# Kernel optimization log

Hardware: AMD Instinct MI355X
Metric: run time of the kernel (lower is better)

## Reference

```python
import jax, jax.numpy as jnp
import numpy as np

D_MODEL = 512
N_HEADS = 8
D_HEAD = D_MODEL // N_HEADS
MAX_LEN = 5000


def _make_pe():
    # sinusoidal table for relative positions -MAX_LEN..+MAX_LEN
    pos = np.arange(-MAX_LEN, MAX_LEN + 1, dtype=np.float32)[:, None]
    div = np.exp(np.arange(0, D_MODEL, 2, dtype=np.float32) * (-np.log(10000.0) / D_MODEL))
    pe = np.zeros((2 * MAX_LEN + 1, D_MODEL), dtype=np.float32)
    pe[:, 0::2] = np.sin(pos * div)
    pe[:, 1::2] = np.cos(pos * div)
    return jnp.asarray(pe)


def setup_inputs() -> dict:
    key = jax.random.key(0)
    ks = jax.random.split(key, 10)
    B, S = 8, 512
    xavier = lambda k: jax.random.uniform(k, (D_MODEL, D_MODEL), jnp.float32,
                                          -np.sqrt(6.0 / (2 * D_MODEL)), np.sqrt(6.0 / (2 * D_MODEL)))
    return {
        "x": jax.random.normal(ks[0], (B, S, D_MODEL), jnp.float32),
        "wq": xavier(ks[1]), "bq": jnp.zeros((D_MODEL,), jnp.float32),
        "wk": xavier(ks[2]), "bk": jnp.zeros((D_MODEL,), jnp.float32),
        "wv": xavier(ks[3]), "bv": jnp.zeros((D_MODEL,), jnp.float32),
        "wo": xavier(ks[4]), "bo": jnp.zeros((D_MODEL,), jnp.float32),
        "wr": xavier(ks[5]),
        "u": jnp.zeros((N_HEADS, D_HEAD), jnp.float32),
        "v_bias": jnp.zeros((N_HEADS, D_HEAD), jnp.float32),
        "pe": _make_pe(),
    }


def reference(x, wq, bq, wk, bk, wv, bv, wo, bo, wr, u, v_bias, pe):
    B, S, D = x.shape
    H, dh = N_HEADS, D_HEAD
    scale = dh ** -0.5

    # projections (torch Linear: x @ W.T + b) -> [B, H, S, dh]
    def proj(w, b):
        return (x @ w.T + b).reshape(B, S, H, dh).transpose(0, 2, 1, 3)
    q = proj(wq, bq)
    k = proj(wk, bk)
    v = proj(wv, bv)

    # relative position encodings: rel[i,j] = pe[clip(j-i) + MAX_LEN]
    pos = jnp.arange(S)
    rel_idx = jnp.clip(pos[None, :] - pos[:, None], -MAX_LEN, MAX_LEN) + MAX_LEN
    rel_pos = pe[rel_idx]                              # [S, S, D]
    rel_proj = (rel_pos @ wr.T).reshape(S, S, H, dh)   # [S, S, H, dh]
    rel_proj = rel_proj.transpose(2, 0, 1, 3)          # [H, S, S, dh]

    content = jnp.einsum('bhid,bhjd->bhij', q + u[None, :, None, :], k)
    position = jnp.einsum('bhid,hijd->bhij', q + v_bias[None, :, None, :], rel_proj)
    attn = jax.nn.softmax((content + position) * scale, axis=-1)

    out = jnp.einsum('bhij,bhjd->bhid', attn, v)       # [B, H, S, dh]
    out = out.transpose(0, 2, 1, 3).reshape(B, S, D)
    return out @ wo.T + bo
```

## Files before the change

### kernel.cpp

```cpp
#include <hip/hip_runtime.h>
#include <math.h>

#define DM 512
#define NH 8
#define DH 64
#define SEQ 512
#define BATCH 8
#define MR 1023
#define PE_OFF 4489

typedef float4 f4;
typedef __attribute__((ext_vector_type(8))) short bf16x8;
typedef __attribute__((ext_vector_type(4))) float f32x4;
typedef __attribute__((ext_vector_type(8))) unsigned short u16x8;
typedef __attribute__((ext_vector_type(4))) unsigned short u16x4;

__device__ __forceinline__ unsigned short f2bf(float f) {
    unsigned x = __float_as_uint(f);
    unsigned r = x + 0x7fffu + ((x >> 16) & 1u);
    return (unsigned short)(r >> 16);
}
__device__ __forceinline__ float bf2f(unsigned short h) {
    return __uint_as_float(((unsigned)h) << 16);
}
__device__ __forceinline__ f32x4 mfma16(bf16x8 a, bf16x8 b, f32x4 c) {
    return __builtin_amdgcn_mfma_f32_16x16x32_bf16(a, b, c, 0, 0, 0);
}

__device__ __forceinline__ void cvt8(const float* __restrict__ src,
                                     unsigned short* __restrict__ hi,
                                     unsigned short* __restrict__ lo, int i) {
    f4 a = *(const f4*)&src[i];
    f4 b = *(const f4*)&src[i + 4];
    float v[8] = {a.x, a.y, a.z, a.w, b.x, b.y, b.z, b.w};
    u16x8 h, l;
#pragma unroll
    for (int j = 0; j < 8; ++j) {
        unsigned short hb = f2bf(v[j]);
        h[j] = hb;
        l[j] = f2bf(v[j] - bf2f(hb));
    }
    *(u16x8*)&hi[i] = h;
    *(u16x8*)&lo[i] = l;
}

__global__ __launch_bounds__(256) void cvt_all_kernel(
    const float* __restrict__ x,
    const float* __restrict__ w0, const float* __restrict__ w1,
    const float* __restrict__ w2, const float* __restrict__ w3,
    const float* __restrict__ w4, const float* __restrict__ pe,
    unsigned short* __restrict__ xh, unsigned short* __restrict__ xl,
    unsigned short* __restrict__ wb,
    unsigned short* __restrict__ peh, unsigned short* __restrict__ pel)
{
    const int bid = blockIdx.x, tid = threadIdx.x;
    if (bid < 1024) {
        cvt8(x, xh, xl, (bid * 256 + tid) * 8);
    } else if (bid < 1664) {
        const int wsel = (bid - 1024) >> 7;
        const float* src = (wsel == 0) ? w0 : (wsel == 1) ? w1 :
                           (wsel == 2) ? w2 : (wsel == 3) ? w3 : w4;
        unsigned short* hi = wb + (size_t)wsel * 524288;
        cvt8(src, hi, hi + 262144, (((bid - 1024) & 127) * 256 + tid) * 8);
    } else {
        const int i = ((bid - 1664) * 256 + tid) * 8;
        if (i < 523776) cvt8(pe, peh, pel, i);
    }
}

__device__ __forceinline__ void gemm_core128(
    const unsigned short* __restrict__ Ah, const unsigned short* __restrict__ Al,
    const unsigned short* __restrict__ Wh, const unsigned short* __restrict__ Wl,
    int m0, int n0, f32x4 acc[4][2],
    unsigned short* LAh, unsigned short* LAl,
    unsigned short* LBh, unsigned short* LBl)
{
    const int tid = threadIdx.x;
    const int lane = tid & 63, wid = tid >> 6;
    const int wm = (wid >> 1) << 6, wn = (wid & 1) << 5;
    const int ar = tid >> 1, ac = (tid & 1) << 4;
    const int br = tid >> 2, bc = (tid & 3) << 3;
    const int fr = lane & 15, g = lane >> 4;

#pragma unroll
    for (int i = 0; i < 4; ++i)
#pragma unroll
        for (int j = 0; j < 2; ++j)
            acc[i][j] = (f32x4){0.f, 0.f, 0.f, 0.f};

    const size_t arow = (size_t)(m0 + ar) * DM + ac;
    const size_t wrow = (size_t)(n0 + br) * DM + bc;

    for (int k0 = 0; k0 < DM; k0 += 32) {
        u16x8 a0 = *(const u16x8*)&Ah[arow + k0];
        u16x8 a1 = *(const u16x8*)&Ah[arow + k0 + 8];
        u16x8 a2 = *(const u16x8*)&Al[arow + k0];
        u16x8 a3 = *(const u16x8*)&Al[arow + k0 + 8];
        u16x8 b0 = *(const u16x8*)&Wh[wrow + k0];
        u16x8 b1 = *(const u16x8*)&Wl[wrow + k0];
        if (k0) __syncthreads();
        *(u16x8*)&LAh[ar * 40 + ac] = a0;
        *(u16x8*)&LAh[ar * 40 + ac + 8] = a1;
        *(u16x8*)&LAl[ar * 40 + ac] = a2;
        *(u16x8*)&LAl[ar * 40 + ac + 8] = a3;
        *(u16x8*)&LBh[br * 40 + bc] = b0;
        *(u16x8*)&LBl[br * 40 + bc] = b1;
        __syncthreads();

        bf16x8 a_h[4], a_l[4], b_h[2], b_l[2];
#pragma unroll
        for (int mi = 0; mi < 4; ++mi) {
            a_h[mi] = *(const bf16x8*)&LAh[(wm + (mi << 4) + fr) * 40 + (g << 3)];
            a_l[mi] = *(const bf16x8*)&LAl[(wm + (mi << 4) + fr) * 40 + (g << 3)];
        }
#pragma unroll
        for (int ni = 0; ni < 2; ++ni) {
            b_h[ni] = *(const bf16x8*)&LBh[(wn + (ni << 4) + fr) * 40 + (g << 3)];
            b_l[ni] = *(const bf16x8*)&LBl[(wn + (ni << 4) + fr) * 40 + (g << 3)];
        }
#pragma unroll
        for (int mi = 0; mi < 4; ++mi)
#pragma unroll
            for (int ni = 0; ni < 2; ++ni) {
                acc[mi][ni] = mfma16(a_h[mi], b_h[ni], acc[mi][ni]);
                acc[mi][ni] = mfma16(a_h[mi], b_l[ni], acc[mi][ni]);
                acc[mi][ni] = mfma16(a_l[mi], b_h[ni], acc[mi][ni]);
            }
    }
}

#define GEMM_LDS \
    __shared__ unsigned short LAh[128 * 40], LAl[128 * 40]; \
    __shared__ unsigned short LBh[64 * 40], LBl[64 * 40];

__global__ __launch_bounds__(256) void qkv_kernel(
    const unsigned short* __restrict__ xh, const unsigned short* __restrict__ xl,
    const unsigned short* __restrict__ wb,
    const float* __restrict__ bq, const float* __restrict__ bk,
    const float* __restrict__ bv, const float* __restrict__ u,
    unsigned short* __restrict__ qh, unsigned short* __restrict__ ql,
    unsigned short* __restrict__ kh, unsigned short* __restrict__ kl,
    unsigned short* __restrict__ vth, unsigned short* __restrict__ vtl)
{
    GEMM_LDS
    const int wsel = blockIdx.x >> 3;
    const int n0 = (blockIdx.x & 7) << 6, m0 = blockIdx.y << 7;
    const unsigned short* Wh = wb + (size_t)wsel * 524288;
    const unsigned short* Wl = Wh + 262144;
    f32x4 acc[4][2];
    gemm_core128(xh, xl, Wh, Wl, m0, n0, acc, LAh, LAl, LBh, LBl);

    const int tid = threadIdx.x, lane = tid & 63, wid = tid >> 6;
    const int wm = (wid >> 1) << 6, wn = (wid & 1) << 5;
    const int fr = lane & 15, g = lane >> 4;
    const float* bias = (wsel == 0) ? bq : (wsel == 1) ? bk : bv;

    if (wsel < 2) {
        unsigned short* oh = (wsel == 0) ? qh : kh;
        unsigned short* ol = (wsel == 0) ? ql : kl;
#pragma unroll
        for (int ni = 0; ni < 2; ++ni) {
            const int n_g = n0 + wn + (ni << 4) + fr;
            float bvv = bias[n_g] + ((wsel == 0) ? u[n_g] : 0.f);
            const int h = n_g >> 6, d = n_g & 63;
#pragma unroll
            for (int mi = 0; mi < 4; ++mi)
#pragma unroll
                for (int r = 0; r < 4; ++r) {
                    const int m_g = m0 + wm + (mi << 4) + (g << 2) + r;
                    const int b = m_g >> 9, s = m_g & 511;
                    const float val = acc[mi][ni][r] + bvv;
                    const size_t o = ((size_t)(b * NH + h) * SEQ + s) * DH + d;
                    const unsigned short hb = f2bf(val);
                    oh[o] = hb;
                    ol[o] = f2bf(val - bf2f(hb));
                }
        }
    } else {
#pragma unroll
        for (int ni = 0; ni < 2; ++ni) {
            const int n_g = n0 + wn + (ni << 4) + fr;
            const float bvv = bias[n_g];
            const int h = n_g >> 6, d = n_g & 63;
#pragma unroll
            for (int mi = 0; mi < 4; ++mi) {
                const int m_b = m0 + wm + (mi << 4) + (g << 2);
                const int b = m_b >> 9, s = m_b & 511;
                u16x4 hv, lv;
#pragma unroll
                for (int r = 0; r < 4; ++r) {
                    const float val = acc[mi][ni][r] + bvv;
                    hv[r] = f2bf(val);
                    lv[r] = f2bf(val - bf2f(hv[r]));
                }
                const size_t o = ((size_t)(b * NH + h) * DH + d) * SEQ + s;
                *(u16x4*)&vth[o] = hv;
                *(u16x4*)&vtl[o] = lv;
            }
        }
    }
}

__global__ __launch_bounds__(256) void rm_kernel(
    const unsigned short* __restrict__ peh, const unsigned short* __restrict__ pel,
    const unsigned short* __restrict__ wrh, const unsigned short* __restrict__ wrl,
    const float* __restrict__ u, const float* __restrict__ vb,
    unsigned short* __restrict__ rmh, unsigned short* __restrict__ rml,
    float* __restrict__ rc)
{
    GEMM_LDS
    const int n0 = blockIdx.x << 6, m0 = blockIdx.y << 7;
    f32x4 acc[4][2];
    gemm_core128(peh, pel, wrh, wrl, m0, n0, acc, LAh, LAl, LBh, LBl);

    const int tid = threadIdx.x, lane = tid & 63, wid = tid >> 6;
    const int wm = (wid >> 1) << 6, wn = (wid & 1) << 5;
    const int fr = lane & 15, g = lane >> 4;
    const int h = n0 >> 6;

    float part[4][4];
    float wgt[2];
#pragma unroll
    for (int ni = 0; ni < 2; ++ni) {
        const int d = wn + (ni << 4) + fr;
        wgt[ni] = vb[(h << 6) + d] - u[(h << 6) + d];
    }
#pragma unroll
    for (int mi = 0; mi < 4; ++mi)
#pragma unroll
        for (int r = 0; r < 4; ++r) part[mi][r] = 0.f;

#pragma unroll
    for (int ni = 0; ni < 2; ++ni) {
        const int n_g = n0 + wn + (ni << 4) + fr;
        const int d = n_g & 63;
#pragma unroll
        for (int mi = 0; mi < 4; ++mi)
#pragma unroll
            for (int r = 0; r < 4; ++r) {
                const int dd = m0 + wm + (mi << 4) + (g << 2) + r;
                const float val = acc[mi][ni][r];
                const size_t o = (((size_t)h << 10) + dd) * DH + d;
                const unsigned short hb = f2bf(val);
                rmh[o] = hb;
                rml[o] = f2bf(val - bf2f(hb));
                part[mi][r] = fmaf(wgt[ni], val, part[mi][r]);
            }
    }

    __syncthreads();
    float* cbuf = (float*)LAh;
#pragma unroll
    for (int mi = 0; mi < 4; ++mi)
#pragma unroll
        for (int r = 0; r < 4; ++r) {
            float v = part[mi][r];
#pragma unroll
            for (int off = 8; off; off >>= 1) v += __shfl_xor(v, off, 16);
            if (fr == 0)
                cbuf[((wid & 1) << 7) + wm + (mi << 4) + (g << 2) + r] = v;
        }
    __syncthreads();
    if (tid < 128)
        rc[((size_t)h << 10) + m0 + tid] = cbuf[tid] + cbuf[128 + tid];
}

__global__ __launch_bounds__(256) void out_kernel(
    const unsigned short* __restrict__ cth, const unsigned short* __restrict__ ctl,
    const unsigned short* __restrict__ woh, const unsigned short* __restrict__ wol,
    const float* __restrict__ bo, float* __restrict__ out)
{
    GEMM_LDS
    const int n0 = blockIdx.x << 6, m0 = blockIdx.y << 7;
    f32x4 acc[4][2];
    gemm_core128(cth, ctl, woh, wol, m0, n0, acc, LAh, LAl, LBh, LBl);

    const int tid = threadIdx.x, lane = tid & 63, wid = tid >> 6;
    const int wm = (wid >> 1) << 6, wn = (wid & 1) << 5;
    const int fr = lane & 15, g = lane >> 4;
#pragma unroll
    for (int ni = 0; ni < 2; ++ni) {
        const int n_g = n0 + wn + (ni << 4) + fr;
        const float bvv = bo[n_g];
#pragma unroll
        for (int mi = 0; mi < 4; ++mi)
#pragma unroll
            for (int r = 0; r < 4; ++r) {
                const int m_g = m0 + wm + (mi << 4) + (g << 2) + r;
                out[(size_t)m_g * DM + n_g] = acc[mi][ni][r] + bvv;
            }
    }
}

__global__ __launch_bounds__(256) void attn_kernel(
    const unsigned short* __restrict__ qh_g, const unsigned short* __restrict__ ql_g,
    const unsigned short* __restrict__ kh_g, const unsigned short* __restrict__ kl_g,
    const unsigned short* __restrict__ vh_g, const unsigned short* __restrict__ vl_g,
    const unsigned short* __restrict__ rmh, const unsigned short* __restrict__ rml,
    const float* __restrict__ rc,
    unsigned short* __restrict__ cth, unsigned short* __restrict__ ctl)
{
    __shared__ unsigned short Kh[64][72], Kl[64][72], Vh[64][72], Vl[64][72];
    __shared__ unsigned short Pdd[4][16][84];
    __shared__ unsigned short Pth[4][16][72];

    const int tid = threadIdx.x;
    const int lane = tid & 63, wid = tid >> 6;
    const int g = lane >> 4, c = lane & 15;
    const int i0 = blockIdx.x << 6;
    const int h = blockIdx.y, b = blockIdx.z;
    const int R0 = i0 + (wid << 4);
    const size_t bh = (size_t)(b * NH + h) * (SEQ * DH);

    const int srow = tid >> 3;
    const int sch = (tid & 7) << 3;

    bf16x8 qhf[2], qlf[2];
#pragma unroll
    for (int ks = 0; ks < 2; ++ks) {
        const size_t qo = bh + (size_t)(R0 + c) * DH + (ks << 5) + (g << 3);
        qhf[ks] = *(const bf16x8*)&qh_g[qo];
        qlf[ks] = *(const bf16x8*)&ql_g[qo];
    }

    f32x4 Oacc[4];
#pragma unroll
    for (int nf = 0; nf < 4; ++nf) Oacc[nf] = (f32x4){0.f, 0.f, 0.f, 0.f};
    float m_r[4] = {-3e38f, -3e38f, -3e38f, -3e38f};
    float l_r[4] = {0.f, 0.f, 0.f, 0.f};

    const float* rch = rc + (h << 10);
    const unsigned short* rmhh = rmh + ((size_t)h << 16);
    const unsigned short* rmlh = rml + ((size_t)h << 16);

    u16x8 p0, p1, p2, p3, p4, p5, p6, p7;
    {
        const size_t kb = bh + (size_t)srow * DH + sch;
        p0 = *(const u16x8*)&kh_g[kb];
        p1 = *(const u16x8*)&kh_g[kb + 32 * DH];
        p2 = *(const u16x8*)&kl_g[kb];
        p3 = *(const u16x8*)&kl_g[kb + 32 * DH];
        const size_t vb_ = bh + (size_t)srow * SEQ + sch;
        p4 = *(const u16x8*)&vh_g[vb_];
        p5 = *(const u16x8*)&vh_g[vb_ + 32 * SEQ];
        p6 = *(const u16x8*)&vl_g[vb_];
        p7 = *(const u16x8*)&vl_g[vb_ + 32 * SEQ];
    }

    for (int jt = 0; jt < 8; ++jt) {
        const int j0 = jt << 6;
        __syncthreads();
        *(u16x8*)&Kh[srow][sch] = p0;
        *(u16x8*)&Kh[srow + 32][sch] = p1;
        *(u16x8*)&Kl[srow][sch] = p2;
        *(u16x8*)&Kl[srow + 32][sch] = p3;
        *(u16x8*)&Vh[srow][sch] = p4;
        *(u16x8*)&Vh[srow + 32][sch] = p5;
        *(u16x8*)&Vl[srow][sch] = p6;
        *(u16x8*)&Vl[srow + 32][sch] = p7;
        __syncthreads();
        if (jt < 7) {
            const int jn = j0 + 64;
            const size_t kb = bh + (size_t)(jn + srow) * DH + sch;
            p0 = *(const u16x8*)&kh_g[kb];
            p1 = *(const u16x8*)&kh_g[kb + 32 * DH];
            p2 = *(const u16x8*)&kl_g[kb];
            p3 = *(const u16x8*)&kl_g[kb + 32 * DH];
            const size_t vb_ = bh + (size_t)srow * SEQ + jn + sch;
            p4 = *(const u16x8*)&vh_g[vb_];
            p5 = *(const u16x8*)&vh_g[vb_ + 32 * SEQ];
            p6 = *(const u16x8*)&vl_g[vb_];
            p7 = *(const u16x8*)&vl_g[vb_ + 32 * SEQ];
        }

        __builtin_amdgcn_s_setprio(1);
        f32x4 accs[4];
#pragma unroll
        for (int nf = 0; nf < 4; ++nf) accs[nf] = (f32x4){0.f, 0.f, 0.f, 0.f};
#pragma unroll
        for (int ks = 0; ks < 2; ++ks)
#pragma unroll
            for (int nf = 0; nf < 4; ++nf) {
                bf16x8 b_h = *(const bf16x8*)&Kh[(nf << 4) + c][(ks << 5) + (g << 3)];
                bf16x8 b_l = *(const bf16x8*)&Kl[(nf << 4) + c][(ks << 5) + (g << 3)];
                accs[nf] = mfma16(qhf[ks], b_h, accs[nf]);
                accs[nf] = mfma16(qhf[ks], b_l, accs[nf]);
                accs[nf] = mfma16(qlf[ks], b_h, accs[nf]);
            }

        const int base_g = j0 - R0 + 496;
#pragma unroll
        for (int f = 0; f < 5; ++f) {
            f32x4 ap = (f32x4){0.f, 0.f, 0.f, 0.f};
#pragma unroll
            for (int ks = 0; ks < 2; ++ks) {
                const size_t ro = (size_t)(base_g + (f << 4) + c) * DH
                                + (ks << 5) + (g << 3);
                bf16x8 b_h = *(const bf16x8*)&rmhh[ro];
                bf16x8 b_l = *(const bf16x8*)&rmlh[ro];
                ap = mfma16(qhf[ks], b_h, ap);
                ap = mfma16(qhf[ks], b_l, ap);
                ap = mfma16(qlf[ks], b_h, ap);
            }
            const float rcv = rch[base_g + (f << 4) + c];
#pragma unroll
            for (int r = 0; r < 4; ++r)
                Pdd[wid][(g << 2) + r][(f << 4) + c] = f2bf(ap[r] + rcv);
        }
        __builtin_amdgcn_s_setprio(0);

#pragma unroll
        for (int r = 0; r < 4; ++r) {
            const int irow = (g << 2) + r;
            float sc[4];
#pragma unroll
            for (int nf = 0; nf < 4; ++nf) {
                const int ddl = (nf << 4) + c - irow + 15;
                sc[nf] = (accs[nf][r] + bf2f(Pdd[wid][irow][ddl])) * 0.125f;
            }
            float mt = fmaxf(fmaxf(sc[0], sc[1]), fmaxf(sc[2], sc[3]));
#pragma unroll
            for (int off = 8; off; off >>= 1) mt = fmaxf(mt, __shfl_xor(mt, off, 16));
            const float mn = fmaxf(m_r[r], mt);
            const float alpha = __expf(m_r[r] - mn);
            m_r[r] = mn;
            float rs = 0.f;
#pragma unroll
            for (int nf = 0; nf < 4; ++nf) {
                const float p = __expf(sc[nf] - mn);
                Pth[wid][irow][(nf << 4) + c] = f2bf(p);
                rs += p;
            }
#pragma unroll
            for (int off = 8; off; off >>= 1) rs += __shfl_xor(rs, off, 16);
            l_r[r] = l_r[r] * alpha + rs;
#pragma unroll
            for (int nf = 0; nf < 4; ++nf) Oacc[nf][r] *= alpha;
        }

        __builtin_amdgcn_s_setprio(1);
#pragma unroll
        for (int ks = 0; ks < 2; ++ks) {
            bf16x8 ph = *(const bf16x8*)&Pth[wid][c][(ks << 5) + (g << 3)];
#pragma unroll
            for (int nf = 0; nf < 4; ++nf) {
                bf16x8 v_h = *(const bf16x8*)&Vh[(nf << 4) + c][(ks << 5) + (g << 3)];
                bf16x8 v_l = *(const bf16x8*)&Vl[(nf << 4) + c][(ks << 5) + (g << 3)];
                Oacc[nf] = mfma16(ph, v_h, Oacc[nf]);
                Oacc[nf] = mfma16(ph, v_l, Oacc[nf]);
            }
        }
        __builtin_amdgcn_s_setprio(0);
    }

    float inv[4];
#pragma unroll
    for (int r = 0; r < 4; ++r) inv[r] = 1.f / l_r[r];
#pragma unroll
    for (int nf = 0; nf < 4; ++nf)
#pragma unroll
        for (int r = 0; r < 4; ++r) {
            const float val = Oacc[nf][r] * inv[r];
            const int s = R0 + (g << 2) + r;
            const int d = (h << 6) + (nf << 4) + c;
            const size_t o = ((size_t)(b * SEQ) + s) * DM + d;
            const unsigned short hb = f2bf(val);
            cth[o] = hb;
            ctl[o] = f2bf(val - bf2f(hb));
        }
}

extern "C" void kernel_launch(void* const* d_in, const int* in_sizes, int n_in,
                              void* d_out, int out_size, void* d_ws, size_t ws_size,
                              hipStream_t stream)
{
    const float* x  = (const float*)d_in[0];
    const float* wq = (const float*)d_in[1];
    const float* bq = (const float*)d_in[2];
    const float* wk = (const float*)d_in[3];
    const float* bk = (const float*)d_in[4];
    const float* wv = (const float*)d_in[5];
    const float* bv = (const float*)d_in[6];
    const float* wo = (const float*)d_in[7];
    const float* bo = (const float*)d_in[8];
    const float* wr = (const float*)d_in[9];
    const float* u  = (const float*)d_in[10];
    const float* vb = (const float*)d_in[11];
    const float* pe = (const float*)d_in[12];
    float* out = (float*)d_out;
    unsigned short* us = (unsigned short*)d_ws;

    unsigned short* xh  = us;
    unsigned short* xl  = us + 2097152;
    unsigned short* wb  = us + 4194304;
    unsigned short* peh = us + 6815744;
    unsigned short* pel = us + 7340032;
    unsigned short* qh  = us + 7864320;
    unsigned short* ql  = us + 9961472;
    unsigned short* kh  = us + 12058624;
    unsigned short* kl  = us + 14155776;
    unsigned short* vth = us + 16252928;
    unsigned short* vtl = us + 18350080;
    unsigned short* rmh = us + 20447232;
    unsigned short* rml = us + 20971520;
    unsigned short* cth = us + 21495808;
    unsigned short* ctl = us + 23592960;
    float* rc = (float*)(us + 25690112);

    unsigned short* woh = wb + 3 * 524288;
    unsigned short* wol = woh + 262144;
    unsigned short* wrh = wb + 4 * 524288;
    unsigned short* wrl = wrh + 262144;

    dim3 blk(256);
    cvt_all_kernel<<<1920, blk, 0, stream>>>(x, wq, wk, wv, wo, wr,
                                             pe + (size_t)PE_OFF * DM,
                                             xh, xl, wb, peh, pel);
    qkv_kernel<<<dim3(24, 32), blk, 0, stream>>>(xh, xl, wb, bq, bk, bv, u,
                                                 qh, ql, kh, kl, vth, vtl);
    rm_kernel<<<dim3(8, 8), blk, 0, stream>>>(peh, pel, wrh, wrl, u, vb,
                                              rmh, rml, rc);
    attn_kernel<<<dim3(8, 8, 8), blk, 0, stream>>>(qh, ql, kh, kl, vth, vtl,
                                                   rmh, rml, rc, cth, ctl);
    out_kernel<<<dim3(8, 32), blk, 0, stream>>>(cth, ctl, woh, wol, bo, out);
}
```

Baseline: 127.6 us.

## Fuse QKV and relative-position projections into one launch; split P into hi/lo for PV

Merges the relative-position projection GEMM into the QKV projection kernel as extra blocks of a single grid, removing a separate launch and letting the small rm GEMM overlap with QKV work. Separately, the attention kernel now keeps softmax probabilities in fp32 shared memory and splits them into bf16 hi/lo parts, adding a third MFMA per PV step for better precision. The precision change adds MFMA work, conversion ALU and LDS usage in the attention inner loop.

```diff
diff --git a/kernel.cpp b/kernel.cpp
--- a/kernel.cpp
+++ b/kernel.cpp
@@ -133,26 +133,90 @@
     __shared__ unsigned short LAh[128 * 40], LAl[128 * 40]; \
     __shared__ unsigned short LBh[64 * 40], LBl[64 * 40];
 
-__global__ __launch_bounds__(256) void qkv_kernel(
+__global__ __launch_bounds__(256) void qkv_rm_kernel(
     const unsigned short* __restrict__ xh, const unsigned short* __restrict__ xl,
     const unsigned short* __restrict__ wb,
+    const unsigned short* __restrict__ peh, const unsigned short* __restrict__ pel,
     const float* __restrict__ bq, const float* __restrict__ bk,
     const float* __restrict__ bv, const float* __restrict__ u,
+    const float* __restrict__ vb,
     unsigned short* __restrict__ qh, unsigned short* __restrict__ ql,
     unsigned short* __restrict__ kh, unsigned short* __restrict__ kl,
-    unsigned short* __restrict__ vth, unsigned short* __restrict__ vtl)
+    unsigned short* __restrict__ vth, unsigned short* __restrict__ vtl,
+    unsigned short* __restrict__ rmh, unsigned short* __restrict__ rml,
+    float* __restrict__ rc)
 {
     GEMM_LDS
-    const int wsel = blockIdx.x >> 3;
-    const int n0 = (blockIdx.x & 7) << 6, m0 = blockIdx.y << 7;
+    const int bid = blockIdx.x;
+    const int tid = threadIdx.x, lane = tid & 63, wid = tid >> 6;
+    const int wm = (wid >> 1) << 6, wn = (wid & 1) << 5;
+    const int fr = lane & 15, g = lane >> 4;
+
+    if (bid < 64) {
+        const int n0 = (bid & 7) << 6, m0 = (bid >> 3) << 7;
+        const unsigned short* wrh = wb + 4 * 524288;
+        const unsigned short* wrl = wrh + 262144;
+        f32x4 acc[4][2];
+        gemm_core128(peh, pel, wrh, wrl, m0, n0, acc, LAh, LAl, LBh, LBl);
+
+        const int h = n0 >> 6;
+        float part[4][4];
+        float wgt[2];
+#pragma unroll
+        for (int ni = 0; ni < 2; ++ni) {
+            const int d = wn + (ni << 4) + fr;
+            wgt[ni] = vb[(h << 6) + d] - u[(h << 6) + d];
+        }
+#pragma unroll
+        for (int mi = 0; mi < 4; ++mi)
+#pragma unroll
+            for (int r = 0; r < 4; ++r) part[mi][r] = 0.f;
+
+#pragma unroll
+        for (int ni = 0; ni < 2; ++ni) {
+            const int n_g = n0 + wn + (ni << 4) + fr;
+            const int d = n_g & 63;
+#pragma unroll
+            for (int mi = 0; mi < 4; ++mi)
+#pragma unroll
+                for (int r = 0; r < 4; ++r) {
+                    const int dd = m0 + wm + (mi << 4) + (g << 2) + r;
+                    const float val = acc[mi][ni][r];
+                    const size_t o = (((size_t)h << 10) + dd) * DH + d;
+                    const unsigned short hb = f2bf(val);
+                    rmh[o] = hb;
+                    rml[o] = f2bf(val - bf2f(hb));
+                    part[mi][r] = fmaf(wgt[ni], val, part[mi][r]);
+                }
+        }
+
+        __syncthreads();
+        float* cbuf = (float*)LAh;
+#pragma unroll
+        for (int mi = 0; mi < 4; ++mi)
+#pragma unroll
+            for (int r = 0; r < 4; ++r) {
+                float v = part[mi][r];
+#pragma unroll
+                for (int off = 8; off; off >>= 1) v += __shfl_xor(v, off, 16);
+                if (fr == 0)
+                    cbuf[((wid & 1) << 7) + wm + (mi << 4) + (g << 2) + r] = v;
+            }
+        __syncthreads();
+        if (tid < 128)
+            rc[((size_t)h << 10) + m0 + tid] = cbuf[tid] + cbuf[128 + tid];
+        return;
+    }
+
+    const int t = bid - 64;
+    const int wsel = t >> 8;
+    const int rest = t & 255;
+    const int n0 = (rest & 7) << 6, m0 = (rest >> 3) << 7;
     const unsigned short* Wh = wb + (size_t)wsel * 524288;
     const unsigned short* Wl = Wh + 262144;
     f32x4 acc[4][2];
     gemm_core128(xh, xl, Wh, Wl, m0, n0, acc, LAh, LAl, LBh, LBl);
 
-    const int tid = threadIdx.x, lane = tid & 63, wid = tid >> 6;
-    const int wm = (wid >> 1) << 6, wn = (wid & 1) << 5;
-    const int fr = lane & 15, g = lane >> 4;
     const float* bias = (wsel == 0) ? bq : (wsel == 1) ? bk : bv;
 
     if (wsel < 2) {
@@ -199,70 +263,6 @@
             }
         }
     }
-}
-
-__global__ __launch_bounds__(256) void rm_kernel(
-    const unsigned short* __restrict__ peh, const unsigned short* __restrict__ pel,
-    const unsigned short* __restrict__ wrh, const unsigned short* __restrict__ wrl,
-    const float* __restrict__ u, const float* __restrict__ vb,
-    unsigned short* __restrict__ rmh, unsigned short* __restrict__ rml,
-    float* __restrict__ rc)
-{
-    GEMM_LDS
-    const int n0 = blockIdx.x << 6, m0 = blockIdx.y << 7;
-    f32x4 acc[4][2];
-    gemm_core128(peh, pel, wrh, wrl, m0, n0, acc, LAh, LAl, LBh, LBl);
-
-    const int tid = threadIdx.x, lane = tid & 63, wid = tid >> 6;
-    const int wm = (wid >> 1) << 6, wn = (wid & 1) << 5;
-    const int fr = lane & 15, g = lane >> 4;
-    const int h = n0 >> 6;
-
-    float part[4][4];
-    float wgt[2];
-#pragma unroll
-    for (int ni = 0; ni < 2; ++ni) {
-        const int d = wn + (ni << 4) + fr;
-        wgt[ni] = vb[(h << 6) + d] - u[(h << 6) + d];
-    }
-#pragma unroll
-    for (int mi = 0; mi < 4; ++mi)
-#pragma unroll
-        for (int r = 0; r < 4; ++r) part[mi][r] = 0.f;
-
-#pragma unroll
-    for (int ni = 0; ni < 2; ++ni) {
-        const int n_g = n0 + wn + (ni << 4) + fr;
-        const int d = n_g & 63;
-#pragma unroll
-        for (int mi = 0; mi < 4; ++mi)
-#pragma unroll
-            for (int r = 0; r < 4; ++r) {
-                const int dd = m0 + wm + (mi << 4) + (g << 2) + r;
-                const float val = acc[mi][ni][r];
-                const size_t o = (((size_t)h << 10) + dd) * DH + d;
-                const unsigned short hb = f2bf(val);
-                rmh[o] = hb;
-                rml[o] = f2bf(val - bf2f(hb));
-                part[mi][r] = fmaf(wgt[ni], val, part[mi][r]);
-            }
-    }
-
-    __syncthreads();
-    float* cbuf = (float*)LAh;
-#pragma unroll
-    for (int mi = 0; mi < 4; ++mi)
-#pragma unroll
-        for (int r = 0; r < 4; ++r) {
-            float v = part[mi][r];
-#pragma unroll
-            for (int off = 8; off; off >>= 1) v += __shfl_xor(v, off, 16);
-            if (fr == 0)
-                cbuf[((wid & 1) << 7) + wm + (mi << 4) + (g << 2) + r] = v;
-        }
-    __syncthreads();
-    if (tid < 128)
-        rc[((size_t)h << 10) + m0 + tid] = cbuf[tid] + cbuf[128 + tid];
 }
 
 __global__ __launch_bounds__(256) void out_kernel(
@@ -302,7 +302,7 @@
 {
     __shared__ unsigned short Kh[64][72], Kl[64][72], Vh[64][72], Vl[64][72];
     __shared__ unsigned short Pdd[4][16][84];
-    __shared__ unsigned short Pth[4][16][72];
+    __shared__ float Pt[4][16][68];
 
     const int tid = threadIdx.x;
     const int lane = tid & 63, wid = tid >> 6;
@@ -428,7 +428,7 @@
 #pragma unroll
             for (int nf = 0; nf < 4; ++nf) {
                 const float p = __expf(sc[nf] - mn);
-                Pth[wid][irow][(nf << 4) + c] = f2bf(p);
+                Pt[wid][irow][(nf << 4) + c] = p;
                 rs += p;
             }
 #pragma unroll
@@ -441,13 +441,23 @@
         __builtin_amdgcn_s_setprio(1);
 #pragma unroll
         for (int ks = 0; ks < 2; ++ks) {
-            bf16x8 ph = *(const bf16x8*)&Pth[wid][c][(ks << 5) + (g << 3)];
+            f4 pv0 = *(const f4*)&Pt[wid][c][(ks << 5) + (g << 3)];
+            f4 pv1 = *(const f4*)&Pt[wid][c][(ks << 5) + (g << 3) + 4];
+            float pv[8] = {pv0.x, pv0.y, pv0.z, pv0.w, pv1.x, pv1.y, pv1.z, pv1.w};
+            bf16x8 ph, pl;
+#pragma unroll
+            for (int e = 0; e < 8; ++e) {
+                const unsigned short hb = f2bf(pv[e]);
+                ph[e] = (short)hb;
+                pl[e] = (short)f2bf(pv[e] - bf2f(hb));
+            }
 #pragma unroll
             for (int nf = 0; nf < 4; ++nf) {
                 bf16x8 v_h = *(const bf16x8*)&Vh[(nf << 4) + c][(ks << 5) + (g << 3)];
                 bf16x8 v_l = *(const bf16x8*)&Vl[(nf << 4) + c][(ks << 5) + (g << 3)];
                 Oacc[nf] = mfma16(ph, v_h, Oacc[nf]);
                 Oacc[nf] = mfma16(ph, v_l, Oacc[nf]);
+                Oacc[nf] = mfma16(pl, v_h, Oacc[nf]);
             }
         }
         __builtin_amdgcn_s_setprio(0);
@@ -509,17 +519,15 @@
 
     unsigned short* woh = wb + 3 * 524288;
     unsigned short* wol = woh + 262144;
-    unsigned short* wrh = wb + 4 * 524288;
-    unsigned short* wrl = wrh + 262144;
 
     dim3 blk(256);
     cvt_all_kernel<<<1920, blk, 0, stream>>>(x, wq, wk, wv, wo, wr,
                                              pe + (size_t)PE_OFF * DM,
                                              xh, xl, wb, peh, pel);
-    qkv_kernel<<<dim3(24, 32), blk, 0, stream>>>(xh, xl, wb, bq, bk, bv, u,
-                                                 qh, ql, kh, kl, vth, vtl);
-    rm_kernel<<<dim3(8, 8), blk, 0, stream>>>(peh, pel, wrh, wrl, u, vb,
-                                              rmh, rml, rc);
+    qkv_rm_kernel<<<832, blk, 0, stream>>>(xh, xl, wb, peh, pel,
+                                           bq, bk, bv, u, vb,
+                                           qh, ql, kh, kl, vth, vtl,
+                                           rmh, rml, rc);
     attn_kernel<<<dim3(8, 8, 8), blk, 0, stream>>>(qh, ql, kh, kl, vth, vtl,
                                                    rmh, rml, rc, cth, ctl);
     out_kernel<<<dim3(8, 32), blk, 0, stream>>>(cth, ctl, woh, wol, bo, out);
```

Measured after the change: 125.0 us. 1.02x faster.
